# Optimization experiments

Measured on AMD Instinct MI355X. Metric: run time of the kernel, lower is better.

The kernel has to match this reference:

```python
import jax, jax.numpy as jnp
import numpy as np

B, S, H = 2, 2048, 1024
NUM_HEAD = 16
HEAD_HIDDEN = H // NUM_HEAD
SCALE = float(np.sqrt(HEAD_HIDDEN))  # 8.0
INF = 10000000000.0


def setup_inputs() -> dict:
    key = jax.random.key(0)
    ks = jax.random.split(key, 12)
    std = 1.0 / np.sqrt(H)
    mk = lambda k: (jax.random.normal(k, (H, H), jnp.float32) * std)
    return {
        "query": jax.random.normal(ks[0], (B, S, H), jnp.float32),
        "key": jax.random.normal(ks[1], (B, S, H), jnp.float32),
        "value": jax.random.normal(ks[2], (B, S, H), jnp.float32),
        "att_mask": jnp.ones((B, 1, 1, S), jnp.float32),
        "wq": mk(ks[3]), "bq": jnp.zeros((H,), jnp.float32),
        "wk": mk(ks[4]), "bk": jnp.zeros((H,), jnp.float32),
        "wv": mk(ks[5]), "bv": jnp.zeros((H,), jnp.float32),
        "wo": mk(ks[6]), "bo": jnp.zeros((H,), jnp.float32),
    }


def reference(query, key, value, att_mask, wq, bq, wk, bk, wv, bv, wo, bo):
    # projections (weights stored as [in, out])
    q = query @ wq + bq
    k = key @ wk + bk
    v = value @ wv + bv
    # split heads: [B, S, nH, hd]
    q = q.reshape(B, S, NUM_HEAD, HEAD_HIDDEN)
    k = k.reshape(B, S, NUM_HEAD, HEAD_HIDDEN)
    v = v.reshape(B, S, NUM_HEAD, HEAD_HIDDEN)
    # scores [B, nH, Sq, Sk], first divide by scale
    att = jnp.einsum("bqhd,bkhd->bhqk", q, k) / SCALE
    # additive mask applied BEFORE the second scale division (faithful quirk)
    att = att + (1.0 - att_mask) * (-INF)
    att = jax.nn.softmax(att / SCALE, axis=-1)
    out = jnp.einsum("bhqk,bkhd->bqhd", att, v).reshape(B, S, H)
    return out @ wo + bo
```

## Files before the change

kernel.cpp:

```cpp
#include <hip/hip_runtime.h>
#include <cstdint>

typedef unsigned short u16;
typedef __attribute__((ext_vector_type(8))) short bf16x8;
typedef __attribute__((ext_vector_type(4))) short bf16x4;
typedef __attribute__((ext_vector_type(4))) float f32x4;

#define S_LEN 2048
#define HDIM  1024
#define NHEAD 16

__device__ __forceinline__ float bf2f(u16 u){ return __uint_as_float(((uint32_t)u) << 16); }
__device__ __forceinline__ u16 f2bf(float f){
  uint32_t x = __float_as_uint(f);
  return (u16)((x + 0x7fffu + ((x >> 16) & 1u)) >> 16);
}

__device__ __forceinline__ void gload_lds16(const void* g, void* l){
  __builtin_amdgcn_global_load_lds((const __attribute__((address_space(1))) void*)g,
                                   (__attribute__((address_space(3))) void*)l, 16, 0, 0);
}

__global__ __launch_bounds__(256) void k_cvt3(const float* __restrict__ q, const float* __restrict__ k,
                                              const float* __restrict__ v, u16* __restrict__ oq,
                                              u16* __restrict__ ok, u16* __restrict__ ov){
  int z = blockIdx.y;
  const float* in = z == 0 ? q : (z == 1 ? k : v);
  u16* out = z == 0 ? oq : (z == 1 ? ok : ov);
  int i = blockIdx.x * 256 + threadIdx.x;
  float4 f0 = *(const float4*)&in[(size_t)i * 8];
  float4 f1 = *(const float4*)&in[(size_t)i * 8 + 4];
  bf16x8 o;
  o[0] = (short)f2bf(f0.x); o[1] = (short)f2bf(f0.y);
  o[2] = (short)f2bf(f0.z); o[3] = (short)f2bf(f0.w);
  o[4] = (short)f2bf(f1.x); o[5] = (short)f2bf(f1.y);
  o[6] = (short)f2bf(f1.z); o[7] = (short)f2bf(f1.w);
  *(bf16x8*)&out[(size_t)i * 8] = o;
}

__global__ __launch_bounds__(256) void k_tr_w4(const float* __restrict__ w0, const float* __restrict__ w1,
                                               const float* __restrict__ w2, const float* __restrict__ w3,
                                               u16* __restrict__ o0, u16* __restrict__ o1,
                                               u16* __restrict__ o2, u16* __restrict__ o3){
  int z = blockIdx.z;
  const float* in = z == 0 ? w0 : (z == 1 ? w1 : (z == 2 ? w2 : w3));
  u16* out = z == 0 ? o0 : (z == 1 ? o1 : (z == 2 ? o2 : o3));
  __shared__ float t[64][65];
  int r0 = threadIdx.x >> 6;
  int c  = threadIdx.x & 63;
  int bx = blockIdx.x * 64, by = blockIdx.y * 64;
  #pragma unroll
  for (int i = 0; i < 64; i += 4) t[r0 + i][c] = in[(size_t)(by + r0 + i) * 1024 + bx + c];
  __syncthreads();
  #pragma unroll
  for (int i = 0; i < 64; i += 4) out[(size_t)(bx + r0 + i) * 1024 + by + c] = f2bf(t[c][r0 + i]);
}

__global__ __launch_bounds__(256) void k_tr_v(const u16* __restrict__ v, u16* __restrict__ vt){
  __shared__ u16 t[64][65];
  int r0 = threadIdx.x >> 6, c = threadIdx.x & 63;
  int s0 = blockIdx.x * 64;
  int bh = blockIdx.y;
  int b = bh >> 4, h = bh & 15;
  const u16* src = v + (size_t)b * S_LEN * HDIM + h * 64;
  #pragma unroll
  for (int i = 0; i < 64; i += 4) t[r0 + i][c] = src[(size_t)(s0 + r0 + i) * HDIM + c];
  __syncthreads();
  u16* dst = vt + (size_t)bh * 64 * S_LEN + s0;
  #pragma unroll
  for (int i = 0; i < 64; i += 4) dst[(size_t)(r0 + i) * S_LEN + c] = t[c][r0 + i];
}

__global__ __launch_bounds__(256) void k_gemm_qkv(const u16* __restrict__ A0, const u16* __restrict__ A1,
                                                  const u16* __restrict__ A2,
                                                  const u16* __restrict__ W0, const u16* __restrict__ W1,
                                                  const u16* __restrict__ W2,
                                                  const float* __restrict__ b0, const float* __restrict__ b1,
                                                  const float* __restrict__ b2,
                                                  u16* __restrict__ C0, u16* __restrict__ C1,
                                                  u16* __restrict__ C2)
{
  int z = blockIdx.z;
  const u16* A  = z == 0 ? A0 : (z == 1 ? A1 : A2);
  const u16* Wt = z == 0 ? W0 : (z == 1 ? W1 : W2);
  const float* bias = z == 0 ? b0 : (z == 1 ? b1 : b2);
  u16* C = z == 0 ? C0 : (z == 1 ? C1 : C2);
  float scale = z == 0 ? (1.0f / 64.0f) : 1.0f;

  __shared__ u16 As[128 * 32];
  __shared__ u16 Bs[128 * 32];
  const int K = 1024, N = 1024;
  int tid = threadIdx.x;
  int lane = tid & 63, wave = tid >> 6;
  int quad = lane >> 4, c16 = lane & 15;
  int wm = wave >> 1, wn = wave & 1;
  int m0 = blockIdx.x * 128, n0 = blockIdx.y * 128;

  f32x4 acc[4][4] = {};

  for (int k0 = 0; k0 < K; k0 += 32) {
    #pragma unroll
    for (int i = 0; i < 2; i++) {
      int slot = tid + i * 256;
      int r = slot >> 2, cc = (slot & 3) * 8;
      gload_lds16(&A [(size_t)(m0 + r) * K + k0 + cc], &As[slot * 8]);
      gload_lds16(&Wt[(size_t)(n0 + r) * K + k0 + cc], &Bs[slot * 8]);
    }
    __syncthreads();
    bf16x8 af[4], bfr[4];
    #pragma unroll
    for (int mt = 0; mt < 4; mt++) af[mt]  = *(const bf16x8*)&As[(wm * 64 + mt * 16 + c16) * 32 + quad * 8];
    #pragma unroll
    for (int nt = 0; nt < 4; nt++) bfr[nt] = *(const bf16x8*)&Bs[(wn * 64 + nt * 16 + c16) * 32 + quad * 8];
    #pragma unroll
    for (int mt = 0; mt < 4; mt++)
      #pragma unroll
      for (int nt = 0; nt < 4; nt++)
        acc[mt][nt] = __builtin_amdgcn_mfma_f32_16x16x32_bf16(af[mt], bfr[nt], acc[mt][nt], 0, 0, 0);
    __syncthreads();
  }

  #pragma unroll
  for (int nt = 0; nt < 4; nt++) {
    int gc = n0 + wn * 64 + nt * 16 + c16;
    float bv = bias[gc];
    #pragma unroll
    for (int mt = 0; mt < 4; mt++)
      #pragma unroll
      for (int r = 0; r < 4; r++) {
        int gr = m0 + wm * 64 + mt * 16 + quad * 4 + r;
        C[(size_t)gr * N + gc] = f2bf((acc[mt][nt][r] + bv) * scale);
      }
  }
}

__global__ __launch_bounds__(256) void k_gemm_o(const u16* __restrict__ A, const u16* __restrict__ Wt,
                                                const float* __restrict__ bias, float* __restrict__ C)
{
  __shared__ u16 As[128 * 32];
  __shared__ u16 Bs[64 * 32];
  const int K = 1024, N = 1024;
  int tid = threadIdx.x;
  int lane = tid & 63, wave = tid >> 6;
  int quad = lane >> 4, c16 = lane & 15;
  int wm = wave >> 1, wn = wave & 1;
  int m0 = blockIdx.x * 128, n0 = blockIdx.y * 64;

  f32x4 acc[4][2] = {};

  for (int k0 = 0; k0 < K; k0 += 32) {
    #pragma unroll
    for (int i = 0; i < 2; i++) {
      int slot = tid + i * 256;
      int r = slot >> 2, cc = (slot & 3) * 8;
      gload_lds16(&A[(size_t)(m0 + r) * K + k0 + cc], &As[slot * 8]);
    }
    {
      int r = tid >> 2, cc = (tid & 3) * 8;
      gload_lds16(&Wt[(size_t)(n0 + r) * K + k0 + cc], &Bs[tid * 8]);
    }
    __syncthreads();
    bf16x8 af[4], bfr[2];
    #pragma unroll
    for (int mt = 0; mt < 4; mt++) af[mt]  = *(const bf16x8*)&As[(wm * 64 + mt * 16 + c16) * 32 + quad * 8];
    #pragma unroll
    for (int nt = 0; nt < 2; nt++) bfr[nt] = *(const bf16x8*)&Bs[(wn * 32 + nt * 16 + c16) * 32 + quad * 8];
    #pragma unroll
    for (int mt = 0; mt < 4; mt++)
      #pragma unroll
      for (int nt = 0; nt < 2; nt++)
        acc[mt][nt] = __builtin_amdgcn_mfma_f32_16x16x32_bf16(af[mt], bfr[nt], acc[mt][nt], 0, 0, 0);
    __syncthreads();
  }

  #pragma unroll
  for (int nt = 0; nt < 2; nt++) {
    int gc = n0 + wn * 32 + nt * 16 + c16;
    float bv = bias[gc];
    #pragma unroll
    for (int mt = 0; mt < 4; mt++)
      #pragma unroll
      for (int r = 0; r < 4; r++) {
        int gr = m0 + wm * 64 + mt * 16 + quad * 4 + r;
        C[(size_t)gr * N + gc] = acc[mt][nt][r] + bv;
      }
  }
}

__global__ __launch_bounds__(256, 2) void k_attn(const u16* __restrict__ Qm,
                                                 const u16* __restrict__ Km,
                                                 const u16* __restrict__ VTm,
                                                 const float* __restrict__ mask,
                                                 u16* __restrict__ Om)
{
  __shared__ u16 Ks[2][64 * 72];
  __shared__ u16 VTs[2][64 * 72];
  __shared__ float Msall[S_LEN];
  int tid = threadIdx.x;
  int lane = tid & 63, wave = tid >> 6;
  int quad = lane >> 4, c16 = lane & 15;
  int qb = blockIdx.x, h = blockIdx.y, b = blockIdx.z;
  const size_t SH = (size_t)S_LEN * HDIM;
  const u16* Qbase  = Qm + (size_t)b * SH + (size_t)qb * 128 * HDIM + h * 64;
  const u16* Kbase  = Km + (size_t)b * SH + h * 64;
  const u16* VTbase = VTm + (size_t)(b * NHEAD + h) * 64 * S_LEN;
  const float* Mbase = mask + (size_t)b * S_LEN;

  auto stage = [&](int s0, int bb) {
    #pragma unroll
    for (int i = 0; i < 5; i++) {
      int c = i * 256 + tid;
      if (c < 576) {
        int r = c / 9, cc = c - r * 9;
        int col = (cc == 8) ? 0 : cc * 8;
        gload_lds16(&Kbase[(size_t)(s0 + r) * HDIM + col], &Ks[bb][c * 8]);
      } else if (c < 1152) {
        int c2 = c - 576;
        int r = c2 / 9, cc = c2 - r * 9;
        int col = (cc == 8) ? 0 : cc * 8;
        gload_lds16(&VTbase[(size_t)r * S_LEN + s0 + col], &VTs[bb][c2 * 8]);
      }
    }
  };

  for (int i = tid; i < S_LEN; i += 256) Msall[i] = (1.0f - Mbase[i]) * (-1.25e9f);

  int qw0 = wave * 32;

  bf16x8 bq[2][2];
  #pragma unroll
  for (int qt = 0; qt < 2; qt++)
    #pragma unroll
    for (int kk = 0; kk < 2; kk++)
      bq[qt][kk] = *(const bf16x8*)&Qbase[(size_t)(qw0 + qt * 16 + c16) * HDIM + kk * 32 + quad * 8];

  f32x4 oacc[2][4] = {};
  float lsq[2] = {};

  stage(0, 0);
  __syncthreads();

  for (int kt = 0; kt < S_LEN / 64; kt++) {
    int s0 = kt * 64;
    int cb = kt & 1;
    if (kt + 1 < S_LEN / 64) stage(s0 + 64, cb ^ 1);

    f32x4 madd[4];
    #pragma unroll
    for (int kvt = 0; kvt < 4; kvt++) madd[kvt] = *(const f32x4*)&Msall[s0 + kvt * 16 + quad * 4];

    f32x4 sacc[4][2];
    #pragma unroll
    for (int kvt = 0; kvt < 4; kvt++)
      #pragma unroll
      for (int qt = 0; qt < 2; qt++)
        sacc[kvt][qt] = madd[kvt];
    #pragma unroll
    for (int kk = 0; kk < 2; kk++) {
      bf16x8 ak[4];
      #pragma unroll
      for (int kvt = 0; kvt < 4; kvt++)
        ak[kvt] = *(const bf16x8*)&Ks[cb][(kvt * 16 + c16) * 72 + kk * 32 + quad * 8];
      #pragma unroll
      for (int kvt = 0; kvt < 4; kvt++)
        #pragma unroll
        for (int qt = 0; qt < 2; qt++)
          sacc[kvt][qt] = __builtin_amdgcn_mfma_f32_16x16x32_bf16(ak[kvt], bq[qt][kk], sacc[kvt][qt], 0, 0, 0);
    }

    bf16x4 pa[2][4];
    #pragma unroll
    for (int kvt = 0; kvt < 4; kvt++)
      #pragma unroll
      for (int qt = 0; qt < 2; qt++) {
        float p0 = __expf(sacc[kvt][qt][0]);
        float p1 = __expf(sacc[kvt][qt][1]);
        float p2 = __expf(sacc[kvt][qt][2]);
        float p3 = __expf(sacc[kvt][qt][3]);
        lsq[qt] += (p0 + p1) + (p2 + p3);
        union { uint32_t u[2]; bf16x4 v; } cv;
        asm("v_cvt_pk_bf16_f32 %0, %1, %2" : "=v"(cv.u[0]) : "v"(p0), "v"(p1));
        asm("v_cvt_pk_bf16_f32 %0, %1, %2" : "=v"(cv.u[1]) : "v"(p2), "v"(p3));
        pa[qt][kvt] = cv.v;
      }

    #pragma unroll
    for (int kvt = 0; kvt < 4; kvt++) {
      bf16x4 vb[4];
      #pragma unroll
      for (int dt = 0; dt < 4; dt++)
        vb[dt] = *(const bf16x4*)&VTs[cb][(dt * 16 + c16) * 72 + kvt * 16 + quad * 4];
      #pragma unroll
      for (int qt = 0; qt < 2; qt++)
        #pragma unroll
        for (int dt = 0; dt < 4; dt++)
          oacc[qt][dt] = __builtin_amdgcn_mfma_f32_16x16x16bf16_1k(pa[qt][kvt], vb[dt], oacc[qt][dt], 0, 0, 0);
    }
    __syncthreads();
  }

  #pragma unroll
  for (int qt = 0; qt < 2; qt++) {
    float v = lsq[qt];
    v += __shfl_xor(v, 16);
    v += __shfl_xor(v, 32);
    lsq[qt] = v;
  }

  u16* Obase = Om + (size_t)b * SH + (size_t)qb * 128 * HDIM + h * 64;
  #pragma unroll
  for (int qt = 0; qt < 2; qt++)
    #pragma unroll
    for (int r = 0; r < 4; r++) {
      float l = __shfl(lsq[qt], quad * 4 + r);
      float rinv = 1.0f / l;
      int lr = qw0 + qt * 16 + quad * 4 + r;
      #pragma unroll
      for (int dt = 0; dt < 4; dt++)
        Obase[(size_t)lr * HDIM + dt * 16 + c16] = f2bf(oacc[qt][dt][r] * rinv);
    }
}

extern "C" void kernel_launch(void* const* d_in, const int* in_sizes, int n_in,
                              void* d_out, int out_size, void* d_ws, size_t ws_size,
                              hipStream_t stream)
{
  (void)in_sizes; (void)n_in; (void)out_size; (void)ws_size;
  const float* q_in = (const float*)d_in[0];
  const float* k_in = (const float*)d_in[1];
  const float* v_in = (const float*)d_in[2];
  const float* mask = (const float*)d_in[3];
  const float* wq   = (const float*)d_in[4];
  const float* bq   = (const float*)d_in[5];
  const float* wk   = (const float*)d_in[6];
  const float* bk   = (const float*)d_in[7];
  const float* wv   = (const float*)d_in[8];
  const float* bv   = (const float*)d_in[9];
  const float* wo   = (const float*)d_in[10];
  const float* bo   = (const float*)d_in[11];

  u16* ws  = (u16*)d_ws;
  u16* wqt = ws;
  u16* wkt = wqt + (1u << 20);
  u16* wvt = wkt + (1u << 20);
  u16* wot = wvt + (1u << 20);
  u16* qi_ = wot + (1u << 20);
  u16* ki_ = qi_ + (4u << 20);
  u16* vi_ = ki_ + (4u << 20);
  u16* qb_ = vi_ + (4u << 20);
  u16* kb_ = qb_ + (4u << 20);
  u16* vb_ = kb_ + (4u << 20);
  u16* vtb = vb_ + (4u << 20);
  u16* ob_ = vtb + (4u << 20);

  dim3 blk(256);
  k_cvt3<<<dim3(2048, 3), blk, 0, stream>>>(q_in, k_in, v_in, qi_, ki_, vi_);
  k_tr_w4<<<dim3(16, 16, 4), blk, 0, stream>>>(wq, wk, wv, wo, wqt, wkt, wvt, wot);
  k_gemm_qkv<<<dim3(32, 8, 3), blk, 0, stream>>>(qi_, ki_, vi_, wqt, wkt, wvt, bq, bk, bv, qb_, kb_, vb_);
  k_tr_v<<<dim3(32, 32), blk, 0, stream>>>(vb_, vtb);
  k_attn<<<dim3(16, 16, 2), blk, 0, stream>>>(qb_, kb_, vtb, mask, ob_);
  k_gemm_o<<<dim3(32, 16), blk, 0, stream>>>(ob_, wot, bo, (float*)d_out);
}
```

Measured before the change: 227.1 us.

## Halve attention query tile per block and raise occupancy with wave priority hints

The attention kernel now gives each wave 16 query rows instead of 32. The grid doubles to 2048 blocks, and launch bounds ask for 4 blocks per CU. The shared mask buffer is removed: the mask is read from global memory and transformed on each tile, and K/V share one LDS array. s_setprio is added around the MFMA sections to favour matrix issue. The intent is more parallelism and occupancy, at the cost of each K/V tile being reused across half as many queries, which doubles K/V staging traffic.

```diff
diff --git a/kernel.cpp b/kernel.cpp
--- a/kernel.cpp
+++ b/kernel.cpp
@@ -187,21 +187,20 @@
   }
 }
 
-__global__ __launch_bounds__(256, 2) void k_attn(const u16* __restrict__ Qm,
+__global__ __launch_bounds__(256, 4) void k_attn(const u16* __restrict__ Qm,
                                                  const u16* __restrict__ Km,
                                                  const u16* __restrict__ VTm,
                                                  const float* __restrict__ mask,
                                                  u16* __restrict__ Om)
 {
-  __shared__ u16 Ks[2][64 * 72];
-  __shared__ u16 VTs[2][64 * 72];
-  __shared__ float Msall[S_LEN];
+  __shared__ u16 KV[2][9216];
+  const int NT = S_LEN / 64;
   int tid = threadIdx.x;
   int lane = tid & 63, wave = tid >> 6;
   int quad = lane >> 4, c16 = lane & 15;
   int qb = blockIdx.x, h = blockIdx.y, b = blockIdx.z;
   const size_t SH = (size_t)S_LEN * HDIM;
-  const u16* Qbase  = Qm + (size_t)b * SH + (size_t)qb * 128 * HDIM + h * 64;
+  const u16* Qbase  = Qm + (size_t)b * SH + (size_t)qb * 64 * HDIM + h * 64;
   const u16* Kbase  = Km + (size_t)b * SH + h * 64;
   const u16* VTbase = VTm + (size_t)(b * NHEAD + h) * 64 * S_LEN;
   const float* Mbase = mask + (size_t)b * S_LEN;
@@ -213,112 +212,106 @@
       if (c < 576) {
         int r = c / 9, cc = c - r * 9;
         int col = (cc == 8) ? 0 : cc * 8;
-        gload_lds16(&Kbase[(size_t)(s0 + r) * HDIM + col], &Ks[bb][c * 8]);
+        gload_lds16(&Kbase[(size_t)(s0 + r) * HDIM + col], &KV[bb][c * 8]);
       } else if (c < 1152) {
         int c2 = c - 576;
         int r = c2 / 9, cc = c2 - r * 9;
         int col = (cc == 8) ? 0 : cc * 8;
-        gload_lds16(&VTbase[(size_t)r * S_LEN + s0 + col], &VTs[bb][c2 * 8]);
+        gload_lds16(&VTbase[(size_t)r * S_LEN + s0 + col], &KV[bb][4608 + c2 * 8]);
       }
     }
   };
 
-  for (int i = tid; i < S_LEN; i += 256) Msall[i] = (1.0f - Mbase[i]) * (-1.25e9f);
-
-  int qw0 = wave * 32;
-
-  bf16x8 bq[2][2];
-  #pragma unroll
-  for (int qt = 0; qt < 2; qt++)
-    #pragma unroll
-    for (int kk = 0; kk < 2; kk++)
-      bq[qt][kk] = *(const bf16x8*)&Qbase[(size_t)(qw0 + qt * 16 + c16) * HDIM + kk * 32 + quad * 8];
-
-  f32x4 oacc[2][4] = {};
-  float lsq[2] = {};
+  int qw0 = wave * 16;
+
+  bf16x8 bq[2];
+  #pragma unroll
+  for (int kk = 0; kk < 2; kk++)
+    bq[kk] = *(const bf16x8*)&Qbase[(size_t)(qw0 + c16) * HDIM + kk * 32 + quad * 8];
+
+  f32x4 oacc[4] = {};
+  float lsq = 0.0f;
 
   stage(0, 0);
   __syncthreads();
 
-  for (int kt = 0; kt < S_LEN / 64; kt++) {
+  for (int kt = 0; kt < NT; kt++) {
     int s0 = kt * 64;
     int cb = kt & 1;
-    if (kt + 1 < S_LEN / 64) stage(s0 + 64, cb ^ 1);
+    const u16* Kb = &KV[cb][0];
+    const u16* Vb = &KV[cb][4608];
+    if (kt + 1 < NT) stage(s0 + 64, cb ^ 1);
 
     f32x4 madd[4];
     #pragma unroll
-    for (int kvt = 0; kvt < 4; kvt++) madd[kvt] = *(const f32x4*)&Msall[s0 + kvt * 16 + quad * 4];
-
-    f32x4 sacc[4][2];
+    for (int kvt = 0; kvt < 4; kvt++) {
+      f32x4 m = *(const f32x4*)&Mbase[s0 + kvt * 16 + quad * 4];
+      #pragma unroll
+      for (int r = 0; r < 4; r++) madd[kvt][r] = (1.0f - m[r]) * (-1.25e9f);
+    }
+
+    bf16x8 ak0[4], ak1[4];
+    #pragma unroll
+    for (int kvt = 0; kvt < 4; kvt++) {
+      ak0[kvt] = *(const bf16x8*)&Kb[(kvt * 16 + c16) * 72 + quad * 8];
+      ak1[kvt] = *(const bf16x8*)&Kb[(kvt * 16 + c16) * 72 + 32 + quad * 8];
+    }
+    f32x4 sacc[4];
+    __builtin_amdgcn_s_setprio(1);
     #pragma unroll
     for (int kvt = 0; kvt < 4; kvt++)
-      #pragma unroll
-      for (int qt = 0; qt < 2; qt++)
-        sacc[kvt][qt] = madd[kvt];
-    #pragma unroll
-    for (int kk = 0; kk < 2; kk++) {
-      bf16x8 ak[4];
-      #pragma unroll
-      for (int kvt = 0; kvt < 4; kvt++)
-        ak[kvt] = *(const bf16x8*)&Ks[cb][(kvt * 16 + c16) * 72 + kk * 32 + quad * 8];
-      #pragma unroll
-      for (int kvt = 0; kvt < 4; kvt++)
-        #pragma unroll
-        for (int qt = 0; qt < 2; qt++)
-          sacc[kvt][qt] = __builtin_amdgcn_mfma_f32_16x16x32_bf16(ak[kvt], bq[qt][kk], sacc[kvt][qt], 0, 0, 0);
-    }
-
-    bf16x4 pa[2][4];
+      sacc[kvt] = __builtin_amdgcn_mfma_f32_16x16x32_bf16(ak0[kvt], bq[0], madd[kvt], 0, 0, 0);
     #pragma unroll
     for (int kvt = 0; kvt < 4; kvt++)
-      #pragma unroll
-      for (int qt = 0; qt < 2; qt++) {
-        float p0 = __expf(sacc[kvt][qt][0]);
-        float p1 = __expf(sacc[kvt][qt][1]);
-        float p2 = __expf(sacc[kvt][qt][2]);
-        float p3 = __expf(sacc[kvt][qt][3]);
-        lsq[qt] += (p0 + p1) + (p2 + p3);
-        union { uint32_t u[2]; bf16x4 v; } cv;
-        asm("v_cvt_pk_bf16_f32 %0, %1, %2" : "=v"(cv.u[0]) : "v"(p0), "v"(p1));
-        asm("v_cvt_pk_bf16_f32 %0, %1, %2" : "=v"(cv.u[1]) : "v"(p2), "v"(p3));
-        pa[qt][kvt] = cv.v;
-      }
-
+      sacc[kvt] = __builtin_amdgcn_mfma_f32_16x16x32_bf16(ak1[kvt], bq[1], sacc[kvt], 0, 0, 0);
+    __builtin_amdgcn_s_setprio(0);
+
+    bf16x4 pa[4];
+    #pragma unroll
+    for (int kvt = 0; kvt < 4; kvt++) {
+      float p0 = __expf(sacc[kvt][0]);
+      float p1 = __expf(sacc[kvt][1]);
+      float p2 = __expf(sacc[kvt][2]);
+      float p3 = __expf(sacc[kvt][3]);
+      lsq += (p0 + p1) + (p2 + p3);
+      union { uint32_t u[2]; bf16x4 v; } cv;
+      asm("v_cvt_pk_bf16_f32 %0, %1, %2" : "=v"(cv.u[0]) : "v"(p0), "v"(p1));
+      asm("v_cvt_pk_bf16_f32 %0, %1, %2" : "=v"(cv.u[1]) : "v"(p2), "v"(p3));
+      pa[kvt] = cv.v;
+    }
+
+    __builtin_amdgcn_s_setprio(1);
     #pragma unroll
     for (int kvt = 0; kvt < 4; kvt++) {
       bf16x4 vb[4];
       #pragma unroll
       for (int dt = 0; dt < 4; dt++)
-        vb[dt] = *(const bf16x4*)&VTs[cb][(dt * 16 + c16) * 72 + kvt * 16 + quad * 4];
-      #pragma unroll
-      for (int qt = 0; qt < 2; qt++)
-        #pragma unroll
-        for (int dt = 0; dt < 4; dt++)
-          oacc[qt][dt] = __builtin_amdgcn_mfma_f32_16x16x16bf16_1k(pa[qt][kvt], vb[dt], oacc[qt][dt], 0, 0, 0);
-    }
-    __syncthreads();
-  }
-
-  #pragma unroll
-  for (int qt = 0; qt < 2; qt++) {
-    float v = lsq[qt];
+        vb[dt] = *(const bf16x4*)&Vb[(dt * 16 + c16) * 72 + kvt * 16 + quad * 4];
+      #pragma unroll
+      for (int dt = 0; dt < 4; dt++)
+        oacc[dt] = __builtin_amdgcn_mfma_f32_16x16x16bf16_1k(pa[kvt], vb[dt], oacc[dt], 0, 0, 0);
+    }
+    __builtin_amdgcn_s_setprio(0);
+    __syncthreads();
+  }
+
+  {
+    float v = lsq;
     v += __shfl_xor(v, 16);
     v += __shfl_xor(v, 32);
-    lsq[qt] = v;
-  }
-
-  u16* Obase = Om + (size_t)b * SH + (size_t)qb * 128 * HDIM + h * 64;
-  #pragma unroll
-  for (int qt = 0; qt < 2; qt++)
-    #pragma unroll
-    for (int r = 0; r < 4; r++) {
-      float l = __shfl(lsq[qt], quad * 4 + r);
-      float rinv = 1.0f / l;
-      int lr = qw0 + qt * 16 + quad * 4 + r;
-      #pragma unroll
-      for (int dt = 0; dt < 4; dt++)
-        Obase[(size_t)lr * HDIM + dt * 16 + c16] = f2bf(oacc[qt][dt][r] * rinv);
-    }
+    lsq = v;
+  }
+
+  u16* Obase = Om + (size_t)b * SH + (size_t)qb * 64 * HDIM + h * 64;
+  #pragma unroll
+  for (int r = 0; r < 4; r++) {
+    float l = __shfl(lsq, quad * 4 + r);
+    float rinv = 1.0f / l;
+    int lr = qw0 + quad * 4 + r;
+    #pragma unroll
+    for (int dt = 0; dt < 4; dt++)
+      Obase[(size_t)lr * HDIM + dt * 16 + c16] = f2bf(oacc[dt][r] * rinv);
+  }
 }
 
 extern "C" void kernel_launch(void* const* d_in, const int* in_sizes, int n_in,
@@ -358,6 +351,6 @@
   k_tr_w4<<<dim3(16, 16, 4), blk, 0, stream>>>(wq, wk, wv, wo, wqt, wkt, wvt, wot);
   k_gemm_qkv<<<dim3(32, 8, 3), blk, 0, stream>>>(qi_, ki_, vi_, wqt, wkt, wvt, bq, bk, bv, qb_, kb_, vb_);
   k_tr_v<<<dim3(32, 32), blk, 0, stream>>>(vb_, vtb);
-  k_attn<<<dim3(16, 16, 2), blk, 0, stream>>>(qb_, kb_, vtb, mask, ob_);
+  k_attn<<<dim3(32, 16, 2), blk, 0, stream>>>(qb_, kb_, vtb, mask, ob_);
   k_gemm_o<<<dim3(32, 16), blk, 0, stream>>>(ob_, wot, bo, (float*)d_out);
 }
```

New measurement: 239.1 us. 5.3% more time.

## Split attention KV tile across wave pairs, use exp2 with folded log2e, setprio MFMA

Applied to the files above, without the earlier changes.

Waves are now arranged as 2 query groups by 2 KV halves. Each wave handles 64 queries against 32 of the 64 keys per tile, and the two halves' partial outputs and row sums are combined through LDS at the end. This reuses K/V fragments across more query tiles per wave and reduces LDS reads per MFMA. The softmax uses raw v_exp_f32 with log2(e) folded into the Q projection scale and the mask constant, and s_setprio raises priority around the MFMA blocks. The cost is more accumulator registers per wave (4x4 oacc) and an extra LDS reduction and barrier in the epilogue.

```diff
diff --git a/kernel.cpp b/kernel.cpp
--- a/kernel.cpp
+++ b/kernel.cpp
@@ -14,6 +14,10 @@
 __device__ __forceinline__ u16 f2bf(float f){
   uint32_t x = __float_as_uint(f);
   return (u16)((x + 0x7fffu + ((x >> 16) & 1u)) >> 16);
+}
+
+__device__ __forceinline__ float exp2_fast(float x){
+  float r; asm("v_exp_f32 %0, %1" : "=v"(r) : "v"(x)); return r;
 }
 
 __device__ __forceinline__ void gload_lds16(const void* g, void* l){
@@ -85,7 +89,7 @@
   const u16* Wt = z == 0 ? W0 : (z == 1 ? W1 : W2);
   const float* bias = z == 0 ? b0 : (z == 1 ? b1 : b2);
   u16* C = z == 0 ? C0 : (z == 1 ? C1 : C2);
-  float scale = z == 0 ? (1.0f / 64.0f) : 1.0f;
+  float scale = z == 0 ? (1.44269504f / 64.0f) : 1.0f;
 
   __shared__ u16 As[128 * 32];
   __shared__ u16 Bs[128 * 32];
@@ -193,12 +197,13 @@
                                                  const float* __restrict__ mask,
                                                  u16* __restrict__ Om)
 {
-  __shared__ u16 Ks[2][64 * 72];
-  __shared__ u16 VTs[2][64 * 72];
+  __shared__ u16 KV[2][9216];
   __shared__ float Msall[S_LEN];
+  const int NT = S_LEN / 64;
   int tid = threadIdx.x;
   int lane = tid & 63, wave = tid >> 6;
   int quad = lane >> 4, c16 = lane & 15;
+  int wq = wave >> 1, wkv = wave & 1;
   int qb = blockIdx.x, h = blockIdx.y, b = blockIdx.z;
   const size_t SH = (size_t)S_LEN * HDIM;
   const u16* Qbase  = Qm + (size_t)b * SH + (size_t)qb * 128 * HDIM + h * 64;
@@ -213,112 +218,139 @@
       if (c < 576) {
         int r = c / 9, cc = c - r * 9;
         int col = (cc == 8) ? 0 : cc * 8;
-        gload_lds16(&Kbase[(size_t)(s0 + r) * HDIM + col], &Ks[bb][c * 8]);
+        gload_lds16(&Kbase[(size_t)(s0 + r) * HDIM + col], &KV[bb][c * 8]);
       } else if (c < 1152) {
         int c2 = c - 576;
         int r = c2 / 9, cc = c2 - r * 9;
         int col = (cc == 8) ? 0 : cc * 8;
-        gload_lds16(&VTbase[(size_t)r * S_LEN + s0 + col], &VTs[bb][c2 * 8]);
+        gload_lds16(&VTbase[(size_t)r * S_LEN + s0 + col], &KV[bb][4608 + c2 * 8]);
       }
     }
   };
 
-  for (int i = tid; i < S_LEN; i += 256) Msall[i] = (1.0f - Mbase[i]) * (-1.25e9f);
-
-  int qw0 = wave * 32;
-
-  bf16x8 bq[2][2];
-  #pragma unroll
-  for (int qt = 0; qt < 2; qt++)
+  stage(0, 0);
+  for (int i = tid; i < S_LEN; i += 256) Msall[i] = (1.0f - Mbase[i]) * (-1.8033688e9f);
+
+  int qw0 = wq * 64;
+  int kv0 = wkv * 32;
+
+  bf16x8 bq[4][2];
+  #pragma unroll
+  for (int qt = 0; qt < 4; qt++)
     #pragma unroll
     for (int kk = 0; kk < 2; kk++)
       bq[qt][kk] = *(const bf16x8*)&Qbase[(size_t)(qw0 + qt * 16 + c16) * HDIM + kk * 32 + quad * 8];
 
-  f32x4 oacc[2][4] = {};
-  float lsq[2] = {};
-
-  stage(0, 0);
+  f32x4 oacc[4][4] = {};
+  float lsq[4] = {};
+
   __syncthreads();
 
-  for (int kt = 0; kt < S_LEN / 64; kt++) {
+  for (int kt = 0; kt < NT; kt++) {
     int s0 = kt * 64;
     int cb = kt & 1;
-    if (kt + 1 < S_LEN / 64) stage(s0 + 64, cb ^ 1);
-
-    f32x4 madd[4];
-    #pragma unroll
-    for (int kvt = 0; kvt < 4; kvt++) madd[kvt] = *(const f32x4*)&Msall[s0 + kvt * 16 + quad * 4];
-
-    f32x4 sacc[4][2];
-    #pragma unroll
-    for (int kvt = 0; kvt < 4; kvt++)
-      #pragma unroll
-      for (int qt = 0; qt < 2; qt++)
-        sacc[kvt][qt] = madd[kvt];
-    #pragma unroll
-    for (int kk = 0; kk < 2; kk++) {
-      bf16x8 ak[4];
-      #pragma unroll
-      for (int kvt = 0; kvt < 4; kvt++)
-        ak[kvt] = *(const bf16x8*)&Ks[cb][(kvt * 16 + c16) * 72 + kk * 32 + quad * 8];
-      #pragma unroll
-      for (int kvt = 0; kvt < 4; kvt++)
-        #pragma unroll
-        for (int qt = 0; qt < 2; qt++)
-          sacc[kvt][qt] = __builtin_amdgcn_mfma_f32_16x16x32_bf16(ak[kvt], bq[qt][kk], sacc[kvt][qt], 0, 0, 0);
-    }
-
-    bf16x4 pa[2][4];
-    #pragma unroll
-    for (int kvt = 0; kvt < 4; kvt++)
-      #pragma unroll
-      for (int qt = 0; qt < 2; qt++) {
-        float p0 = __expf(sacc[kvt][qt][0]);
-        float p1 = __expf(sacc[kvt][qt][1]);
-        float p2 = __expf(sacc[kvt][qt][2]);
-        float p3 = __expf(sacc[kvt][qt][3]);
+    const u16* Kb = &KV[cb][0];
+    const u16* Vb = &KV[cb][4608];
+    if (kt + 1 < NT) stage(s0 + 64, cb ^ 1);
+
+    f32x4 madd[2];
+    #pragma unroll
+    for (int kv2 = 0; kv2 < 2; kv2++) madd[kv2] = *(const f32x4*)&Msall[s0 + kv0 + kv2 * 16 + quad * 4];
+
+    bf16x8 ak0[2], ak1[2];
+    #pragma unroll
+    for (int kv2 = 0; kv2 < 2; kv2++) {
+      ak0[kv2] = *(const bf16x8*)&Kb[(kv0 + kv2 * 16 + c16) * 72 + quad * 8];
+      ak1[kv2] = *(const bf16x8*)&Kb[(kv0 + kv2 * 16 + c16) * 72 + 32 + quad * 8];
+    }
+    f32x4 sacc[2][4];
+    __builtin_amdgcn_s_setprio(1);
+    #pragma unroll
+    for (int kv2 = 0; kv2 < 2; kv2++)
+      #pragma unroll
+      for (int qt = 0; qt < 4; qt++)
+        sacc[kv2][qt] = __builtin_amdgcn_mfma_f32_16x16x32_bf16(ak0[kv2], bq[qt][0], madd[kv2], 0, 0, 0);
+    #pragma unroll
+    for (int kv2 = 0; kv2 < 2; kv2++)
+      #pragma unroll
+      for (int qt = 0; qt < 4; qt++)
+        sacc[kv2][qt] = __builtin_amdgcn_mfma_f32_16x16x32_bf16(ak1[kv2], bq[qt][1], sacc[kv2][qt], 0, 0, 0);
+    __builtin_amdgcn_s_setprio(0);
+
+    bf16x4 pa[4][2];
+    #pragma unroll
+    for (int kv2 = 0; kv2 < 2; kv2++)
+      #pragma unroll
+      for (int qt = 0; qt < 4; qt++) {
+        float p0 = exp2_fast(sacc[kv2][qt][0]);
+        float p1 = exp2_fast(sacc[kv2][qt][1]);
+        float p2 = exp2_fast(sacc[kv2][qt][2]);
+        float p3 = exp2_fast(sacc[kv2][qt][3]);
         lsq[qt] += (p0 + p1) + (p2 + p3);
         union { uint32_t u[2]; bf16x4 v; } cv;
         asm("v_cvt_pk_bf16_f32 %0, %1, %2" : "=v"(cv.u[0]) : "v"(p0), "v"(p1));
         asm("v_cvt_pk_bf16_f32 %0, %1, %2" : "=v"(cv.u[1]) : "v"(p2), "v"(p3));
-        pa[qt][kvt] = cv.v;
-      }
-
-    #pragma unroll
-    for (int kvt = 0; kvt < 4; kvt++) {
+        pa[qt][kv2] = cv.v;
+      }
+
+    __builtin_amdgcn_s_setprio(1);
+    #pragma unroll
+    for (int kv2 = 0; kv2 < 2; kv2++) {
       bf16x4 vb[4];
       #pragma unroll
       for (int dt = 0; dt < 4; dt++)
-        vb[dt] = *(const bf16x4*)&VTs[cb][(dt * 16 + c16) * 72 + kvt * 16 + quad * 4];
-      #pragma unroll
-      for (int qt = 0; qt < 2; qt++)
+        vb[dt] = *(const bf16x4*)&Vb[(dt * 16 + c16) * 72 + kv0 + kv2 * 16 + quad * 4];
+      #pragma unroll
+      for (int qt = 0; qt < 4; qt++)
         #pragma unroll
         for (int dt = 0; dt < 4; dt++)
-          oacc[qt][dt] = __builtin_amdgcn_mfma_f32_16x16x16bf16_1k(pa[qt][kvt], vb[dt], oacc[qt][dt], 0, 0, 0);
-    }
-    __syncthreads();
-  }
-
-  #pragma unroll
-  for (int qt = 0; qt < 2; qt++) {
+          oacc[qt][dt] = __builtin_amdgcn_mfma_f32_16x16x16bf16_1k(pa[qt][kv2], vb[dt], oacc[qt][dt], 0, 0, 0);
+    }
+    __builtin_amdgcn_s_setprio(0);
+    __syncthreads();
+  }
+
+  #pragma unroll
+  for (int qt = 0; qt < 4; qt++) {
     float v = lsq[qt];
     v += __shfl_xor(v, 16);
     v += __shfl_xor(v, 32);
     lsq[qt] = v;
   }
 
-  u16* Obase = Om + (size_t)b * SH + (size_t)qb * 128 * HDIM + h * 64;
-  #pragma unroll
-  for (int qt = 0; qt < 2; qt++)
-    #pragma unroll
-    for (int r = 0; r < 4; r++) {
-      float l = __shfl(lsq[qt], quad * 4 + r);
-      float rinv = 1.0f / l;
-      int lr = qw0 + qt * 16 + quad * 4 + r;
+  float* Osc = (float*)&KV[0][0];
+  float* Lsc = Msall;
+  if (wkv == 1) {
+    float* Ob = Osc + wq * 4096;
+    #pragma unroll
+    for (int qt = 0; qt < 4; qt++)
       #pragma unroll
       for (int dt = 0; dt < 4; dt++)
-        Obase[(size_t)lr * HDIM + dt * 16 + c16] = f2bf(oacc[qt][dt][r] * rinv);
-    }
+        #pragma unroll
+        for (int r = 0; r < 4; r++)
+          Ob[(qt * 16 + quad * 4 + r) * 64 + dt * 16 + c16] = oacc[qt][dt][r];
+    if (lane < 16)
+      #pragma unroll
+      for (int qt = 0; qt < 4; qt++) Lsc[wq * 64 + qt * 16 + lane] = lsq[qt];
+  }
+  __syncthreads();
+  if (wkv == 0) {
+    float* Ob = Osc + wq * 4096;
+    u16* Obase = Om + (size_t)b * SH + (size_t)qb * 128 * HDIM + h * 64;
+    #pragma unroll
+    for (int qt = 0; qt < 4; qt++)
+      #pragma unroll
+      for (int r = 0; r < 4; r++) {
+        float l = __shfl(lsq[qt], quad * 4 + r) + Lsc[wq * 64 + qt * 16 + quad * 4 + r];
+        float rinv = 1.0f / l;
+        int lr = qw0 + qt * 16 + quad * 4 + r;
+        #pragma unroll
+        for (int dt = 0; dt < 4; dt++) {
+          float o = oacc[qt][dt][r] + Ob[(qt * 16 + quad * 4 + r) * 64 + dt * 16 + c16];
+          Obase[(size_t)lr * HDIM + dt * 16 + c16] = f2bf(o * rinv);
+        }
+      }
+  }
 }
 
 extern "C" void kernel_launch(void* const* d_in, const int* in_sizes, int n_in,
```

After: 226.1 us. Within noise of the previous version (-0.4%).
